# Optimization experiments

Hardware: AMD Instinct MI355X
Metric: run time of the kernel (lower is better)

## Reference

```python
import jax, jax.numpy as jnp
import numpy as np

T, E, H, V, K = 1024, 300, 512, 100000, 12
START, STOP = 10, 11


def setup_inputs() -> dict:
    key = jax.random.key(0)
    ks = jax.random.split(key, 12)
    s = 0.05
    sentence = jax.random.randint(ks[0], (T,), 0, V, dtype=jnp.int32)
    tags = jax.random.randint(ks[1], (T,), 0, START, dtype=jnp.int32)  # real tags only
    word_embeds = jax.random.normal(ks[2], (V, E), jnp.float32) * 0.1

    def lstm_p(k):
        k1, k2 = jax.random.split(k)
        return (jax.random.normal(k1, (4 * H, E), jnp.float32) * s,
                jax.random.normal(k2, (4 * H, H), jnp.float32) * s,
                jnp.zeros(4 * H, jnp.float32), jnp.zeros(4 * H, jnp.float32))

    Wih_f, Whh_f, bih_f, bhh_f = lstm_p(ks[3])
    Wih_b, Whh_b, bih_b, bhh_b = lstm_p(ks[4])
    D = 2 * H
    attn_W = jax.random.normal(ks[5], (D, D), jnp.float32) * s
    attn_b = jnp.zeros(D, jnp.float32)
    h2h1_W = jax.random.normal(ks[6], (D, 2 * D), jnp.float32) * s
    h2h1_b = jnp.zeros(D, jnp.float32)
    tag_W = jax.random.normal(ks[7], (K, D), jnp.float32) * s
    tag_b = jnp.zeros(K, jnp.float32)
    transitions = jax.random.normal(ks[8], (K, K), jnp.float32) * 0.01
    transitions = transitions.at[START, :].set(-10000.0).at[:, STOP].set(-10000.0)
    return dict(sentence=sentence, tags=tags, word_embeds=word_embeds,
                Wih_f=Wih_f, Whh_f=Whh_f, bih_f=bih_f, bhh_f=bhh_f,
                Wih_b=Wih_b, Whh_b=Whh_b, bih_b=bih_b, bhh_b=bhh_b,
                attn_W=attn_W, attn_b=attn_b, h2h1_W=h2h1_W, h2h1_b=h2h1_b,
                tag_W=tag_W, tag_b=tag_b, transitions=transitions)


def _lstm_pass(x, Wih, Whh, bih, bhh):
    # x: [T, E] -> hs: [T, H]   (PyTorch LSTM gate order i,f,g,o)
    xg = x @ Wih.T + bih  # [T, 4H] precomputed input contribution

    def step(carry, g_in):
        h, c = carry
        g = g_in + h @ Whh.T + bhh
        i, f, gg, o = jnp.split(g, 4)
        i = jax.nn.sigmoid(i); f = jax.nn.sigmoid(f)
        gg = jnp.tanh(gg); o = jax.nn.sigmoid(o)
        c = f * c + i * gg
        h = o * jnp.tanh(c)
        return (h, c), h

    init = (jnp.zeros(H, x.dtype), jnp.zeros(H, x.dtype))
    _, hs = jax.lax.scan(step, init, xg)
    return hs


def reference(sentence, tags, word_embeds, Wih_f, Whh_f, bih_f, bhh_f,
              Wih_b, Whh_b, bih_b, bhh_b, attn_W, attn_b,
              h2h1_W, h2h1_b, tag_W, tag_b, transitions):
    x = word_embeds[sentence]                       # [T, E]  (dropout is eval no-op)
    h_fwd = _lstm_pass(x, Wih_f, Whh_f, bih_f, bhh_f)
    h_bwd = _lstm_pass(x[::-1], Wih_b, Whh_b, bih_b, bhh_b)[::-1]
    enc = jnp.concatenate([h_fwd, h_bwd], axis=-1)  # [T, 2H]

    # Attn 'general': energy(t, i) = enc[t] . (W enc[i] + b); vectorized per-timestep loop
    proj = enc @ attn_W.T + attn_b                  # [T, 2H]
    scores = enc @ proj.T                           # [T, T]
    w = jax.nn.softmax(scores, axis=-1)
    ctx = w @ enc                                   # [T, 2H]

    h1 = jnp.tanh(jnp.concatenate([enc, ctx], axis=-1) @ h2h1_W.T + h2h1_b)  # [T, 2H]
    feats = h1 @ tag_W.T + tag_b                    # [T, K]

    # CRF forward algorithm (log partition); transitions[to, from]
    alpha0 = jnp.full((K,), -10000.0, feats.dtype).at[START].set(0.0)

    def crf_step(alpha, feat):
        a = jax.nn.logsumexp(alpha[None, :] + transitions, axis=1) + feat
        return a, None

    alpha, _ = jax.lax.scan(crf_step, alpha0, feats)
    logZ = jax.nn.logsumexp(alpha + transitions[STOP])

    # gold path score (_score_sentence)
    pad_start = jnp.concatenate([jnp.array([START], tags.dtype), tags])
    pad_stop = jnp.concatenate([tags, jnp.array([STOP], tags.dtype)])
    gold = transitions[pad_stop, pad_start].sum() + feats[jnp.arange(T), tags].sum()

    return logZ - gold  # CRF negative log-likelihood for this sentence
```

## Files before the change

kernel.cpp:

```cpp
#include <hip/hip_runtime.h>
#include <hip/hip_fp16.h>

#define T_LEN 1024
#define E_DIM 300
#define H_DIM 512
#define D_DIM 1024
#define K_TAGS 12
#define G4 2048

typedef __attribute__((ext_vector_type(8))) short short8x;
typedef __attribute__((ext_vector_type(4))) float f32x4;

static __device__ __forceinline__ float frcp(float x){ return __builtin_amdgcn_rcpf(x); }
static __device__ __forceinline__ float sigm(float x){ return frcp(1.f + __expf(-x)); }
static __device__ __forceinline__ float ftanh(float x){
  const float e = __expf(2.f * fabsf(x));
  const float t = 1.f - 2.f * frcp(e + 1.f);
  return copysignf(t, x);
}
static __device__ __forceinline__ unsigned short f2b(float f){
  unsigned u = __float_as_uint(f);
  return (unsigned short)((u + 0x7fffu + ((u >> 16) & 1u)) >> 16);
}
static __device__ __forceinline__ uint4 pack8(const float* s){
  uint4 o;
  o.x = (unsigned)f2b(s[0]) | ((unsigned)f2b(s[1]) << 16);
  o.y = (unsigned)f2b(s[2]) | ((unsigned)f2b(s[3]) << 16);
  o.z = (unsigned)f2b(s[4]) | ((unsigned)f2b(s[5]) << 16);
  o.w = (unsigned)f2b(s[6]) | ((unsigned)f2b(s[7]) << 16);
  return o;
}
static __device__ __forceinline__ uint4 pack8u(const unsigned short* s){
  uint4 o;
  o.x = (unsigned)s[0] | ((unsigned)s[1] << 16);
  o.y = (unsigned)s[2] | ((unsigned)s[3] << 16);
  o.z = (unsigned)s[4] | ((unsigned)s[5] << 16);
  o.w = (unsigned)s[6] | ((unsigned)s[7] << 16);
  return o;
}

__global__ void k_gather(const int* __restrict__ sent, const float* __restrict__ we,
                         unsigned short* __restrict__ xh){
  int idx = blockIdx.x*256 + threadIdx.x;
  if (idx < T_LEN*E_DIM){
    int t = idx / E_DIM, e = idx - t*E_DIM;
    xh[idx] = f2b(we[(size_t)sent[t]*E_DIM + e]);
  }
}

__global__ __launch_bounds__(256) void k_cast(const float* __restrict__ src,
                                              unsigned short* __restrict__ dst,
                                              int n4){
  int i = blockIdx.x*256 + threadIdx.x;
  if (i < n4){
    const float4 v = *reinterpret_cast<const float4*>(src + (size_t)i*4);
    ushort2 a, b;
    a.x = f2b(v.x); a.y = f2b(v.y); b.x = f2b(v.z); b.y = f2b(v.w);
    *reinterpret_cast<ushort2*>(dst + (size_t)i*4)     = a;
    *reinterpret_cast<ushort2*>(dst + (size_t)i*4 + 2) = b;
  }
}

__global__ void k_init(unsigned* __restrict__ hbuf, unsigned* __restrict__ rdy){
  int i = blockIdx.x*256 + threadIdx.x;
  if (i < 2048) hbuf[i] = 0u;
  if (i < 32)   rdy[i]  = 0u;
}

__global__ __launch_bounds__(256) void k_gemm_mfma(
    const unsigned short* __restrict__ Ah, int lda,
    const unsigned short* __restrict__ Bh, int ldb,
    const float* __restrict__ bias, int act,
    void* __restrict__ Cp, int ldc, int cbf16, int M, int N, int K)
{
  __shared__ __align__(16) unsigned short As[64*40];
  __shared__ __align__(16) unsigned short Bs[64*40];
  const int tid = threadIdx.x;
  const int bm = blockIdx.y*64, bn = blockIdx.x*64;
  const int r  = tid >> 2, c8 = (tid & 3) * 8;
  const int wave = tid >> 6, lane = tid & 63;
  const int wm = (wave >> 1) * 32, wn = (wave & 1) * 32;
  const int col = lane & 15, quad = lane >> 4;

  const unsigned short* arow = Ah + (size_t)(bm+r)*lda;
  const unsigned short* brow = Bh + (size_t)(bn+r)*ldb;

  uint4* aw = (uint4*)(As + r*40 + c8);
  uint4* bw = (uint4*)(Bs + r*40 + c8);

  f32x4 acc[2][2];
  #pragma unroll
  for (int i=0;i<2;i++)
    #pragma unroll
    for (int j=0;j<2;j++) acc[i][j] = (f32x4){0.f,0.f,0.f,0.f};

  for (int k0 = 0; k0 < K; k0 += 32){
    uint4 avv, bvv;
    if (k0 + 32 <= K){
      avv = *(const uint4*)(arow + k0 + c8);
      bvv = *(const uint4*)(brow + k0 + c8);
    } else {
      unsigned short ta[8], tb[8];
      #pragma unroll
      for (int i=0;i<8;i++){
        const int kk = k0 + c8 + i;
        ta[i] = (kk < K) ? arow[kk] : (unsigned short)0;
        tb[i] = (kk < K) ? brow[kk] : (unsigned short)0;
      }
      avv = pack8u(ta); bvv = pack8u(tb);
    }
    if (k0) __syncthreads();
    *aw = avv; *bw = bvv;
    __syncthreads();
    const short8x a0 = *(const short8x*)(As + (wm+col)*40    + quad*8);
    const short8x a1 = *(const short8x*)(As + (wm+16+col)*40 + quad*8);
    const short8x b0 = *(const short8x*)(Bs + (wn+col)*40    + quad*8);
    const short8x b1 = *(const short8x*)(Bs + (wn+16+col)*40 + quad*8);
    acc[0][0] = __builtin_amdgcn_mfma_f32_16x16x32_bf16(a0, b0, acc[0][0], 0, 0, 0);
    acc[0][1] = __builtin_amdgcn_mfma_f32_16x16x32_bf16(a0, b1, acc[0][1], 0, 0, 0);
    acc[1][0] = __builtin_amdgcn_mfma_f32_16x16x32_bf16(a1, b0, acc[1][0], 0, 0, 0);
    acc[1][1] = __builtin_amdgcn_mfma_f32_16x16x32_bf16(a1, b1, acc[1][1], 0, 0, 0);
  }

  #pragma unroll
  for (int mt=0;mt<2;mt++){
    #pragma unroll
    for (int nt=0;nt<2;nt++){
      const int cc = bn + wn + 16*nt + col;
      const float bs = bias ? bias[cc] : 0.f;
      #pragma unroll
      for (int i=0;i<4;i++){
        const int rr = bm + wm + 16*mt + quad*4 + i;
        float v = acc[mt][nt][i] + bs;
        if (act) v = ftanh(v);
        if (cbf16) ((unsigned short*)Cp)[(size_t)rr*ldc + cc] = f2b(v);
        else       ((float*)Cp)[(size_t)rr*ldc + cc] = v;
      }
    }
  }
}

__global__ __launch_bounds__(256, 1) void k_lstm_fused(
    const float* __restrict__ Whh_f, const float* __restrict__ Whh_b,
    const float* __restrict__ bih_f, const float* __restrict__ bhh_f,
    const float* __restrict__ bih_b, const float* __restrict__ bhh_b,
    float* __restrict__ xg_f, float* __restrict__ xg_b,
    const unsigned short* __restrict__ xh,
    const unsigned short* __restrict__ Wih_fh, const unsigned short* __restrict__ Wih_bh,
    unsigned* __restrict__ hbuf, unsigned* __restrict__ xgReady,
    float* __restrict__ enc)
{
  __shared__ __align__(16) unsigned short As[64*40];
  __shared__ __align__(16) unsigned short Bs[64*40];
  __shared__ __align__(16) unsigned short lds_hb[512];
  __shared__ __align__(16) float raw[64];

  const int tid = threadIdx.x;
  const int wave = tid >> 6, lane = tid & 63;
  const int col = lane & 15, quad = lane >> 4;

  if (blockIdx.x >= 64){
    const int pid = blockIdx.x - 64;
    const int r  = tid >> 2, c8 = (tid & 3) * 8;
    const int wm = (wave >> 1) * 32, wn = (wave & 1) * 32;
    uint4* aw = (uint4*)(As + r*40 + c8);
    uint4* bw = (uint4*)(Bs + r*40 + c8);

    for (int j = pid; j < 1024; j += 192){
      const int bm = j >> 6, rem = j & 63, pdir = rem >> 5, bn = rem & 31;
      const unsigned short* Bh = pdir ? Wih_bh : Wih_fh;
      float* C = pdir ? xg_b : xg_f;
      const int am = pdir ? (1023 - (bm*64 + r)) : (bm*64 + r);
      const unsigned short* arow = xh + (size_t)am*E_DIM;
      const unsigned short* brow = Bh + (size_t)(bn*64 + r)*E_DIM;

      f32x4 acc[2][2];
      #pragma unroll
      for (int i=0;i<2;i++)
        #pragma unroll
        for (int jj=0;jj<2;jj++) acc[i][jj] = (f32x4){0.f,0.f,0.f,0.f};

      for (int k0 = 0; k0 < E_DIM; k0 += 32){
        uint4 avv, bvv;
        if (k0 + 32 <= E_DIM){
          avv = *(const uint4*)(arow + k0 + c8);
          bvv = *(const uint4*)(brow + k0 + c8);
        } else {
          unsigned short ta[8], tb[8];
          #pragma unroll
          for (int i=0;i<8;i++){
            const int kk = k0 + c8 + i;
            ta[i] = (kk < E_DIM) ? arow[kk] : (unsigned short)0;
            tb[i] = (kk < E_DIM) ? brow[kk] : (unsigned short)0;
          }
          avv = pack8u(ta); bvv = pack8u(tb);
        }
        __syncthreads();
        *aw = avv; *bw = bvv;
        __syncthreads();
        const short8x a0 = *(const short8x*)(As + (wm+col)*40    + quad*8);
        const short8x a1 = *(const short8x*)(As + (wm+16+col)*40 + quad*8);
        const short8x b0 = *(const short8x*)(Bs + (wn+col)*40    + quad*8);
        const short8x b1 = *(const short8x*)(Bs + (wn+16+col)*40 + quad*8);
        acc[0][0] = __builtin_amdgcn_mfma_f32_16x16x32_bf16(a0, b0, acc[0][0], 0, 0, 0);
        acc[0][1] = __builtin_amdgcn_mfma_f32_16x16x32_bf16(a0, b1, acc[0][1], 0, 0, 0);
        acc[1][0] = __builtin_amdgcn_mfma_f32_16x16x32_bf16(a1, b0, acc[1][0], 0, 0, 0);
        acc[1][1] = __builtin_amdgcn_mfma_f32_16x16x32_bf16(a1, b1, acc[1][1], 0, 0, 0);
      }
      #pragma unroll
      for (int mt=0;mt<2;mt++)
        #pragma unroll
        for (int nt=0;nt<2;nt++)
          #pragma unroll
          for (int i=0;i<4;i++)
            C[(size_t)(bm*64 + wm + 16*mt + quad*4 + i)*G4 + (bn*64 + wn + 16*nt + col)]
              = acc[mt][nt][i];
      __syncthreads();
      if (tid == 0)
        __hip_atomic_fetch_add(&xgReady[pdir*16 + bm], 1u,
                               __ATOMIC_RELEASE, __HIP_MEMORY_SCOPE_AGENT);
    }
    return;
  }

  const int dir = blockIdx.x >> 5;
  const int w   = blockIdx.x & 31;

  const float* Whh = dir ? Whh_b : Whh_f;
  const float* xg  = dir ? xg_b  : xg_f;
  unsigned* rdy = xgReady + dir*16;

  const int rowA = wave*H_DIM + w*16 + col;
  short8x w_frag[16];
  #pragma unroll
  for (int s=0;s<16;s++){
    const float* bp = Whh + (size_t)rowA*H_DIM + s*32 + quad*8;
    uint4 u = pack8(bp);
    w_frag[s] = *reinterpret_cast<short8x*>(&u);
  }

  float bias_r = 0.f, xg_cur = 0.f, c_reg = 0.f;
  int row2 = 0, readyBlk = 0;
  if (tid < 64){
    row2 = (tid >> 4)*H_DIM + w*16 + (tid & 15);
    bias_r = dir ? (bih_b[row2] + bhh_b[row2]) : (bih_f[row2] + bhh_f[row2]);
    while (__hip_atomic_load(rdy, __ATOMIC_RELAXED, __HIP_MEMORY_SCOPE_AGENT) != 32u) {}
    (void)__hip_atomic_load(rdy, __ATOMIC_ACQUIRE, __HIP_MEMORY_SCOPE_AGENT);
    readyBlk = 1;
    xg_cur = xg[row2];
  }

  unsigned* hb = hbuf + dir*1024;

  for (int t = 1; t <= T_LEN; ++t){
    {
      unsigned* s0 = hb + ((t-1)&1)*512 + tid;
      const unsigned want = (unsigned)(t-1);
      unsigned v0 = __hip_atomic_load(s0,     __ATOMIC_RELAXED, __HIP_MEMORY_SCOPE_AGENT);
      unsigned v1 = __hip_atomic_load(s0+256, __ATOMIC_RELAXED, __HIP_MEMORY_SCOPE_AGENT);
      while (((v0 >> 16) != want) || ((v1 >> 16) != want)){
        v0 = __hip_atomic_load(s0,     __ATOMIC_RELAXED, __HIP_MEMORY_SCOPE_AGENT);
        v1 = __hip_atomic_load(s0+256, __ATOMIC_RELAXED, __HIP_MEMORY_SCOPE_AGENT);
      }
      lds_hb[tid]     = (unsigned short)(v0 & 0xffffu);
      lds_hb[tid+256] = (unsigned short)(v1 & 0xffffu);
    }
    __syncthreads();

    float xg_nxt = 0.f;
    if (tid < 64 && t < T_LEN){
      const int nb = t >> 6;
      if (nb >= readyBlk){
        while (__hip_atomic_load(rdy + nb, __ATOMIC_RELAXED, __HIP_MEMORY_SCOPE_AGENT) != 32u) {}
        (void)__hip_atomic_load(rdy + nb, __ATOMIC_ACQUIRE, __HIP_MEMORY_SCOPE_AGENT);
        readyBlk = nb + 1;
      }
      xg_nxt = xg[(size_t)t*G4 + row2];
    }

    f32x4 a0 = (f32x4){0.f,0.f,0.f,0.f}, a1 = (f32x4){0.f,0.f,0.f,0.f};
    #pragma unroll
    for (int s=0;s<16;s+=2){
      const short8x b0 = *(const short8x*)(lds_hb + s*32     + quad*8);
      const short8x b1 = *(const short8x*)(lds_hb + (s+1)*32 + quad*8);
      a0 = __builtin_amdgcn_mfma_f32_16x16x32_bf16(w_frag[s],   b0, a0, 0, 0, 0);
      a1 = __builtin_amdgcn_mfma_f32_16x16x32_bf16(w_frag[s+1], b1, a1, 0, 0, 0);
    }
    if (col == 0){
      f32x4 asum = a0 + a1;
      *reinterpret_cast<f32x4*>(raw + wave*16 + quad*4) = asum;
    }
    __syncthreads();

    if (tid < 64){
      float v = raw[tid] + bias_r + xg_cur;
      const float va = ((tid >> 4) == 2) ? ftanh(v) : sigm(v);
      const int l2 = tid & 15;
      const float iv = __shfl(va, l2);
      const float fv = __shfl(va, l2 + 16);
      const float gg = __shfl(va, l2 + 32);
      const float ov = __shfl(va, l2 + 48);
      if (tid < 16){
        c_reg = fv*c_reg + iv*gg;
        const float hh = ov*ftanh(c_reg);
        const int hj = w*16 + tid;
        const unsigned hv = ((unsigned)t << 16) | (unsigned)f2b(hh);
        __hip_atomic_store(hb + (t&1)*512 + hj, hv,
                           __ATOMIC_RELAXED, __HIP_MEMORY_SCOPE_AGENT);
        const int tt = dir ? (T_LEN - t) : (t - 1);
        enc[(size_t)tt*D_DIM + dir*H_DIM + hj] = hh;
      }
      xg_cur = xg_nxt;
    }
    __syncthreads();
  }
}

__global__ __launch_bounds__(256) void k_softmax(float* __restrict__ S,
                                                 unsigned short* __restrict__ Sh){
  float* r = S + (size_t)blockIdx.x*1024;
  unsigned short* rh = Sh + (size_t)blockIdx.x*1024;
  const int tid = threadIdx.x;
  float v[4];
  #pragma unroll
  for (int i=0;i<4;i++) v[i] = r[tid + i*256];
  float m = fmaxf(fmaxf(v[0],v[1]), fmaxf(v[2],v[3]));
  #pragma unroll
  for (int off=32; off>=1; off>>=1) m = fmaxf(m, __shfl_xor(m, off));
  __shared__ float red[4], red2[4];
  const int wid = tid >> 6, lane = tid & 63;
  if (lane == 0) red[wid] = m;
  __syncthreads();
  m = fmaxf(fmaxf(red[0],red[1]), fmaxf(red[2],red[3]));
  float s = 0.f;
  #pragma unroll
  for (int i=0;i<4;i++){ v[i] = __expf(v[i]-m); s += v[i]; }
  #pragma unroll
  for (int off=32; off>=1; off>>=1) s += __shfl_xor(s, off);
  if (lane == 0) red2[wid] = s;
  __syncthreads();
  s = red2[0]+red2[1]+red2[2]+red2[3];
  const float inv = frcp(s);
  #pragma unroll
  for (int i=0;i<4;i++){
    const float o = v[i]*inv;
    r[tid + i*256]  = o;
    rh[tid + i*256] = f2b(o);
  }
}

__global__ __launch_bounds__(256) void k_encprep(const float* __restrict__ src,
                                                 unsigned short* __restrict__ cath,
                                                 unsigned short* __restrict__ encT){
  __shared__ float tile[32][33];
  const int bx = blockIdx.x*32, by = blockIdx.y*32;
  const int tx = threadIdx.x & 31, ty8 = threadIdx.x >> 5;
  #pragma unroll
  for (int i=ty8;i<32;i+=8){
    const float v = src[(size_t)(by+i)*1024 + bx+tx];
    tile[i][tx] = v;
    cath[(size_t)(by+i)*2048 + bx+tx] = f2b(v);
  }
  __syncthreads();
  #pragma unroll
  for (int i=ty8;i<32;i+=8) encT[(size_t)(bx+i)*1024 + by+tx] = f2b(tile[tx][i]);
}

__global__ __launch_bounds__(256) void k_feats(
    const float* __restrict__ h1, const float* __restrict__ tagW,
    const float* __restrict__ tagb, float* __restrict__ feats)
{
  const int t = blockIdx.x;
  const int wave = threadIdx.x >> 6, lane = threadIdx.x & 63;
  const float* hr = h1 + (size_t)t*D_DIM;
  float hv[16];
  #pragma unroll
  for (int i=0;i<16;i++) hv[i] = hr[lane + 64*i];
  #pragma unroll
  for (int j=0;j<3;j++){
    const int tag = wave*3 + j;
    const float* wr = tagW + (size_t)tag*D_DIM;
    float s = 0.f;
    #pragma unroll
    for (int i=0;i<16;i++) s += hv[i]*wr[lane + 64*i];
    #pragma unroll
    for (int off=32; off>=1; off>>=1) s += __shfl_xor(s, off);
    if (lane == 0) feats[(size_t)t*K_TAGS + tag] = s + tagb[tag];
  }
}

__global__ __launch_bounds__(64) void k_crf1(const float* __restrict__ feats,
                                             const float* __restrict__ trans,
                                             float* __restrict__ chunkM){
  const int c = blockIdx.x;
  const int r = threadIdx.x;
  __shared__ float sT[144];
  __shared__ float sF[16*12];
  for (int i=r; i<144; i+=64) sT[i] = trans[i];
  const int t0 = c*16;
  for (int i=r; i<192; i+=64) sF[i] = feats[(size_t)t0*K_TAGS + i];
  __syncthreads();
  if (r < 12){
    float m[12], nm[12];
    #pragma unroll
    for (int k=0;k<12;k++) m[k] = sT[k*12 + r] + sF[k];
    for (int s=1; s<16; ++s){
      #pragma unroll
      for (int i=0;i<12;i++){
        float v[12]; float mx = -1e30f;
        #pragma unroll
        for (int k=0;k<12;k++){ v[k] = sT[i*12+k] + m[k]; mx = fmaxf(mx, v[k]); }
        float ss = 0.f;
        #pragma unroll
        for (int k=0;k<12;k++) ss += __expf(v[k]-mx);
        nm[i] = sF[s*12+i] + mx + __logf(ss);
      }
      #pragma unroll
      for (int i=0;i<12;i++) m[i] = nm[i];
    }
    #pragma unroll
    for (int k=0;k<12;k++) chunkM[c*144 + k*12 + r] = m[k];
  }
}

__global__ __launch_bounds__(128) void k_crf2(const float* __restrict__ chunkM,
                                              const float* __restrict__ feats,
                                              const float* __restrict__ trans,
                                              const int* __restrict__ tags,
                                              float* __restrict__ out){
  const int tid = threadIdx.x, wave = tid >> 6, lane = tid & 63;
  __shared__ float sGold;
  float alpha = (lane == 10) ? 0.f : -10000.f;
  if (wave == 1){
    float g = 0.f;
    for (int i = lane; i <= T_LEN; i += 64){
      const int to = (i < T_LEN) ? tags[i]   : 11;
      const int fr = (i == 0)    ? 10        : tags[i-1];
      g += trans[to*K_TAGS + fr];
      if (i < T_LEN) g += feats[(size_t)i*K_TAGS + tags[i]];
    }
    #pragma unroll
    for (int off=32; off>=1; off>>=1) g += __shfl_xor(g, off);
    if (lane == 0) sGold = g;
  } else {
    float pf[12];
    #pragma unroll
    for (int k=0;k<12;k++) pf[k] = (lane < 12) ? chunkM[lane*12 + k] : 0.f;
    for (int c=0; c<64; ++c){
      float av[12];
      #pragma unroll
      for (int j=0;j<12;j++) av[j] = __shfl(alpha, j);
      float cur[12];
      #pragma unroll
      for (int k=0;k<12;k++) cur[k] = pf[k];
      if (c+1 < 64){
        #pragma unroll
        for (int k=0;k<12;k++)
          pf[k] = (lane < 12) ? chunkM[(c+1)*144 + lane*12 + k] : 0.f;
      }
      if (lane < 12){
        float v[12]; float mx = -1e30f;
        #pragma unroll
        for (int k=0;k<12;k++){ v[k] = cur[k] + av[k]; mx = fmaxf(mx, v[k]); }
        float ss = 0.f;
        #pragma unroll
        for (int k=0;k<12;k++) ss += __expf(v[k]-mx);
        alpha = mx + __logf(ss);
      }
    }
  }
  __syncthreads();
  if (wave == 0){
    float v = (lane < K_TAGS) ? (alpha + trans[11*K_TAGS + lane]) : -1e30f;
    float m = v;
    #pragma unroll
    for (int off=32; off>=1; off>>=1) m = fmaxf(m, __shfl_xor(m, off));
    float e = (lane < K_TAGS) ? __expf(v - m) : 0.f;
    #pragma unroll
    for (int off=32; off>=1; off>>=1) e += __shfl_xor(e, off);
    if (lane == 0) out[0] = (m + __logf(e)) - sGold;
  }
}

extern "C" void kernel_launch(void* const* d_in, const int* in_sizes, int n_in,
                              void* d_out, int out_size, void* d_ws, size_t ws_size,
                              hipStream_t stream)
{
  const int*   sentence = (const int*)d_in[0];
  const int*   tags     = (const int*)d_in[1];
  const float* we       = (const float*)d_in[2];
  const float* Wih_f    = (const float*)d_in[3];
  const float* Whh_f    = (const float*)d_in[4];
  const float* bih_f    = (const float*)d_in[5];
  const float* bhh_f    = (const float*)d_in[6];
  const float* Wih_b    = (const float*)d_in[7];
  const float* Whh_b    = (const float*)d_in[8];
  const float* bih_b    = (const float*)d_in[9];
  const float* bhh_b    = (const float*)d_in[10];
  const float* attn_W   = (const float*)d_in[11];
  const float* attn_b   = (const float*)d_in[12];
  const float* h2h1_W   = (const float*)d_in[13];
  const float* h2h1_b   = (const float*)d_in[14];
  const float* tag_W    = (const float*)d_in[15];
  const float* tag_b    = (const float*)d_in[16];
  const float* trans    = (const float*)d_in[17];
  float* out = (float*)d_out;

  float* ws = (float*)d_ws;
  float* R1 = ws;
  float* R2 = ws + 2097152;
  float* R3 = ws + 4194304;
  float* R4 = ws + 5242880;
  float* feats = ws + 6291456;
  unsigned* hbuf = (unsigned*)(ws + 6303744);

  float* xg_f = R1;
  float* xg_b = R2;
  float* enc  = R3;
  unsigned short* xh      = (unsigned short*)R4;
  unsigned short* Wih_fh  = (unsigned short*)R4 + 307200;
  unsigned short* Wih_bh  = (unsigned short*)R4 + 921600;
  unsigned* xgReady = (unsigned*)feats;
  unsigned short* cath    = (unsigned short*)R1;
  unsigned short* attn_Wh = (unsigned short*)(R1 + 1048576);
  unsigned short* h2h1_Wh = (unsigned short*)R2;
  float* scores = R2 + 1048576;
  unsigned short* encT    = (unsigned short*)R4;
  unsigned short* projh   = (unsigned short*)R4 + 1048576;
  unsigned short* scoresh = (unsigned short*)R3;
  float* h1     = R3;
  float* chunkM = R4;

  k_gather<<<dim3((T_LEN*E_DIM + 255)/256), dim3(256), 0, stream>>>(sentence, we, xh);
  k_init<<<dim3(8), dim3(256), 0, stream>>>(hbuf, xgReady);
  k_cast<<<dim3(600),  dim3(256), 0, stream>>>(Wih_f, Wih_fh, 153600);
  k_cast<<<dim3(600),  dim3(256), 0, stream>>>(Wih_b, Wih_bh, 153600);
  k_lstm_fused<<<dim3(256), dim3(256), 0, stream>>>(Whh_f, Whh_b, bih_f, bhh_f,
      bih_b, bhh_b, xg_f, xg_b, xh, Wih_fh, Wih_bh, hbuf, xgReady, enc);
  k_encprep<<<dim3(32,32), dim3(256), 0, stream>>>(enc, cath, encT);
  k_cast<<<dim3(1024), dim3(256), 0, stream>>>(attn_W, attn_Wh, 262144);
  k_cast<<<dim3(2048), dim3(256), 0, stream>>>(h2h1_W, h2h1_Wh, 524288);
  k_gemm_mfma<<<dim3(16,16), dim3(256), 0, stream>>>(cath, 2048,
      attn_Wh, D_DIM, attn_b, 0, projh, D_DIM, 1, T_LEN, D_DIM, D_DIM);
  k_gemm_mfma<<<dim3(16,16), dim3(256), 0, stream>>>(cath, 2048,
      projh, D_DIM, nullptr, 0, scores, T_LEN, 0, T_LEN, T_LEN, D_DIM);
  k_softmax<<<dim3(1024), dim3(256), 0, stream>>>(scores, scoresh);
  k_gemm_mfma<<<dim3(16,16), dim3(256), 0, stream>>>(scoresh, T_LEN,
      encT, D_DIM, nullptr, 0, cath + 1024, 2048, 1, T_LEN, D_DIM, T_LEN);
  k_gemm_mfma<<<dim3(16,16), dim3(256), 0, stream>>>(cath, 2048,
      h2h1_Wh, 2048, h2h1_b, 1, h1, D_DIM, 0, T_LEN, D_DIM, 2048);
  k_feats<<<dim3(1024), dim3(256), 0, stream>>>(h1, tag_W, tag_b, feats);
  k_crf1<<<dim3(64), dim3(64), 0, stream>>>(feats, trans, chunkM);
  k_crf2<<<dim3(1), dim3(128), 0, stream>>>(chunkM, feats, trans, tags, out);
}
```

Baseline: 1.823 ms.

## Fuse post-LSTM stages into one persistent kernel with grid barriers

The separate gather, cast and init kernels become one pre-pass kernel. All post-LSTM kernels (enc transpose and cast, weight casts, four GEMMs, softmax, tag features, both CRF stages) are merged into one 256-block persistent kernel that uses atomic grid barriers between phases. Barrier counters reuse hbuf, which the LSTM kernel's block 0 resets to zero at the end. This removes about ten kernel launches and their inter-kernel gaps, at the cost of spin-wait barriers and a correctness dependency on all 256 blocks being co-resident.

```diff
diff --git a/kernel.cpp b/kernel.cpp
--- a/kernel.cpp
+++ b/kernel.cpp
@@ -39,104 +39,31 @@
   return o;
 }
 
-__global__ void k_gather(const int* __restrict__ sent, const float* __restrict__ we,
-                         unsigned short* __restrict__ xh){
-  int idx = blockIdx.x*256 + threadIdx.x;
-  if (idx < T_LEN*E_DIM){
-    int t = idx / E_DIM, e = idx - t*E_DIM;
-    xh[idx] = f2b(we[(size_t)sent[t]*E_DIM + e]);
-  }
-}
-
-__global__ __launch_bounds__(256) void k_cast(const float* __restrict__ src,
-                                              unsigned short* __restrict__ dst,
-                                              int n4){
-  int i = blockIdx.x*256 + threadIdx.x;
-  if (i < n4){
-    const float4 v = *reinterpret_cast<const float4*>(src + (size_t)i*4);
+__global__ __launch_bounds__(256) void k_pre(
+    const int* __restrict__ sent, const float* __restrict__ we,
+    unsigned short* __restrict__ xh,
+    const float* __restrict__ Wf, unsigned short* __restrict__ Wfh,
+    const float* __restrict__ Wb, unsigned short* __restrict__ Wbh,
+    unsigned* __restrict__ hbuf, unsigned* __restrict__ rdy)
+{
+  const int i = blockIdx.x*256 + threadIdx.x;
+  if (i < 2048) hbuf[i] = 0u;
+  else if (i < 2080) rdy[i-2048] = 0u;
+  for (int g = i; g < T_LEN*E_DIM; g += 600*256){
+    int t = g / E_DIM, e = g - t*E_DIM;
+    xh[g] = f2b(we[(size_t)sent[t]*E_DIM + e]);
+  }
+  if (i < 153600){
+    const float4 v = *reinterpret_cast<const float4*>(Wf + (size_t)i*4);
     ushort2 a, b;
     a.x = f2b(v.x); a.y = f2b(v.y); b.x = f2b(v.z); b.y = f2b(v.w);
-    *reinterpret_cast<ushort2*>(dst + (size_t)i*4)     = a;
-    *reinterpret_cast<ushort2*>(dst + (size_t)i*4 + 2) = b;
-  }
-}
-
-__global__ void k_init(unsigned* __restrict__ hbuf, unsigned* __restrict__ rdy){
-  int i = blockIdx.x*256 + threadIdx.x;
-  if (i < 2048) hbuf[i] = 0u;
-  if (i < 32)   rdy[i]  = 0u;
-}
-
-__global__ __launch_bounds__(256) void k_gemm_mfma(
-    const unsigned short* __restrict__ Ah, int lda,
-    const unsigned short* __restrict__ Bh, int ldb,
-    const float* __restrict__ bias, int act,
-    void* __restrict__ Cp, int ldc, int cbf16, int M, int N, int K)
-{
-  __shared__ __align__(16) unsigned short As[64*40];
-  __shared__ __align__(16) unsigned short Bs[64*40];
-  const int tid = threadIdx.x;
-  const int bm = blockIdx.y*64, bn = blockIdx.x*64;
-  const int r  = tid >> 2, c8 = (tid & 3) * 8;
-  const int wave = tid >> 6, lane = tid & 63;
-  const int wm = (wave >> 1) * 32, wn = (wave & 1) * 32;
-  const int col = lane & 15, quad = lane >> 4;
-
-  const unsigned short* arow = Ah + (size_t)(bm+r)*lda;
-  const unsigned short* brow = Bh + (size_t)(bn+r)*ldb;
-
-  uint4* aw = (uint4*)(As + r*40 + c8);
-  uint4* bw = (uint4*)(Bs + r*40 + c8);
-
-  f32x4 acc[2][2];
-  #pragma unroll
-  for (int i=0;i<2;i++)
-    #pragma unroll
-    for (int j=0;j<2;j++) acc[i][j] = (f32x4){0.f,0.f,0.f,0.f};
-
-  for (int k0 = 0; k0 < K; k0 += 32){
-    uint4 avv, bvv;
-    if (k0 + 32 <= K){
-      avv = *(const uint4*)(arow + k0 + c8);
-      bvv = *(const uint4*)(brow + k0 + c8);
-    } else {
-      unsigned short ta[8], tb[8];
-      #pragma unroll
-      for (int i=0;i<8;i++){
-        const int kk = k0 + c8 + i;
-        ta[i] = (kk < K) ? arow[kk] : (unsigned short)0;
-        tb[i] = (kk < K) ? brow[kk] : (unsigned short)0;
-      }
-      avv = pack8u(ta); bvv = pack8u(tb);
-    }
-    if (k0) __syncthreads();
-    *aw = avv; *bw = bvv;
-    __syncthreads();
-    const short8x a0 = *(const short8x*)(As + (wm+col)*40    + quad*8);
-    const short8x a1 = *(const short8x*)(As + (wm+16+col)*40 + quad*8);
-    const short8x b0 = *(const short8x*)(Bs + (wn+col)*40    + quad*8);
-    const short8x b1 = *(const short8x*)(Bs + (wn+16+col)*40 + quad*8);
-    acc[0][0] = __builtin_amdgcn_mfma_f32_16x16x32_bf16(a0, b0, acc[0][0], 0, 0, 0);
-    acc[0][1] = __builtin_amdgcn_mfma_f32_16x16x32_bf16(a0, b1, acc[0][1], 0, 0, 0);
-    acc[1][0] = __builtin_amdgcn_mfma_f32_16x16x32_bf16(a1, b0, acc[1][0], 0, 0, 0);
-    acc[1][1] = __builtin_amdgcn_mfma_f32_16x16x32_bf16(a1, b1, acc[1][1], 0, 0, 0);
-  }
-
-  #pragma unroll
-  for (int mt=0;mt<2;mt++){
-    #pragma unroll
-    for (int nt=0;nt<2;nt++){
-      const int cc = bn + wn + 16*nt + col;
-      const float bs = bias ? bias[cc] : 0.f;
-      #pragma unroll
-      for (int i=0;i<4;i++){
-        const int rr = bm + wm + 16*mt + quad*4 + i;
-        float v = acc[mt][nt][i] + bs;
-        if (act) v = ftanh(v);
-        if (cbf16) ((unsigned short*)Cp)[(size_t)rr*ldc + cc] = f2b(v);
-        else       ((float*)Cp)[(size_t)rr*ldc + cc] = v;
-      }
-    }
+    *reinterpret_cast<ushort2*>(Wfh + (size_t)i*4)     = a;
+    *reinterpret_cast<ushort2*>(Wfh + (size_t)i*4 + 2) = b;
+    const float4 u = *reinterpret_cast<const float4*>(Wb + (size_t)i*4);
+    ushort2 c, d;
+    c.x = f2b(u.x); c.y = f2b(u.y); d.x = f2b(u.z); d.y = f2b(u.w);
+    *reinterpret_cast<ushort2*>(Wbh + (size_t)i*4)     = c;
+    *reinterpret_cast<ushort2*>(Wbh + (size_t)i*4 + 2) = d;
   }
 }
 
@@ -314,171 +241,278 @@
     }
     __syncthreads();
   }
-}
-
-__global__ __launch_bounds__(256) void k_softmax(float* __restrict__ S,
-                                                 unsigned short* __restrict__ Sh){
-  float* r = S + (size_t)blockIdx.x*1024;
-  unsigned short* rh = Sh + (size_t)blockIdx.x*1024;
+
+  if (blockIdx.x == 0 && tid < 16)
+    __hip_atomic_store(hbuf + tid, 0u, __ATOMIC_RELAXED, __HIP_MEMORY_SCOPE_AGENT);
+}
+
+static __device__ __forceinline__ void gbar(unsigned* c){
+  __syncthreads();
+  if (threadIdx.x == 0){
+    __hip_atomic_fetch_add(c, 1u, __ATOMIC_RELEASE, __HIP_MEMORY_SCOPE_AGENT);
+    while (__hip_atomic_load(c, __ATOMIC_RELAXED, __HIP_MEMORY_SCOPE_AGENT) != 256u) {}
+    (void)__hip_atomic_load(c, __ATOMIC_ACQUIRE, __HIP_MEMORY_SCOPE_AGENT);
+  }
+  __syncthreads();
+}
+
+static __device__ void gemm_tile(
+    const unsigned short* __restrict__ Ah, int lda,
+    const unsigned short* __restrict__ Bh, int ldb,
+    const float* __restrict__ bias, int act,
+    void* __restrict__ Cp, int ldc, int cbf16, int K, int bm, int bn,
+    unsigned short* As, unsigned short* Bs)
+{
   const int tid = threadIdx.x;
-  float v[4];
+  const int r  = tid >> 2, c8 = (tid & 3) * 8;
+  const int wave = tid >> 6, lane = tid & 63;
+  const int wm = (wave >> 1) * 32, wn = (wave & 1) * 32;
+  const int col = lane & 15, quad = lane >> 4;
+
+  const unsigned short* arow = Ah + (size_t)(bm+r)*lda;
+  const unsigned short* brow = Bh + (size_t)(bn+r)*ldb;
+  uint4* aw = (uint4*)(As + r*40 + c8);
+  uint4* bw = (uint4*)(Bs + r*40 + c8);
+
+  f32x4 acc[2][2];
   #pragma unroll
-  for (int i=0;i<4;i++) v[i] = r[tid + i*256];
-  float m = fmaxf(fmaxf(v[0],v[1]), fmaxf(v[2],v[3]));
+  for (int i=0;i<2;i++)
+    #pragma unroll
+    for (int j=0;j<2;j++) acc[i][j] = (f32x4){0.f,0.f,0.f,0.f};
+
+  for (int k0 = 0; k0 < K; k0 += 32){
+    const uint4 avv = *(const uint4*)(arow + k0 + c8);
+    const uint4 bvv = *(const uint4*)(brow + k0 + c8);
+    __syncthreads();
+    *aw = avv; *bw = bvv;
+    __syncthreads();
+    const short8x a0 = *(const short8x*)(As + (wm+col)*40    + quad*8);
+    const short8x a1 = *(const short8x*)(As + (wm+16+col)*40 + quad*8);
+    const short8x b0 = *(const short8x*)(Bs + (wn+col)*40    + quad*8);
+    const short8x b1 = *(const short8x*)(Bs + (wn+16+col)*40 + quad*8);
+    acc[0][0] = __builtin_amdgcn_mfma_f32_16x16x32_bf16(a0, b0, acc[0][0], 0, 0, 0);
+    acc[0][1] = __builtin_amdgcn_mfma_f32_16x16x32_bf16(a0, b1, acc[0][1], 0, 0, 0);
+    acc[1][0] = __builtin_amdgcn_mfma_f32_16x16x32_bf16(a1, b0, acc[1][0], 0, 0, 0);
+    acc[1][1] = __builtin_amdgcn_mfma_f32_16x16x32_bf16(a1, b1, acc[1][1], 0, 0, 0);
+  }
+
   #pragma unroll
-  for (int off=32; off>=1; off>>=1) m = fmaxf(m, __shfl_xor(m, off));
+  for (int mt=0;mt<2;mt++){
+    #pragma unroll
+    for (int nt=0;nt<2;nt++){
+      const int cc = bn + wn + 16*nt + col;
+      const float bs = bias ? bias[cc] : 0.f;
+      #pragma unroll
+      for (int i=0;i<4;i++){
+        const int rr = bm + wm + 16*mt + quad*4 + i;
+        float v = acc[mt][nt][i] + bs;
+        if (act) v = ftanh(v);
+        if (cbf16) ((unsigned short*)Cp)[(size_t)rr*ldc + cc] = f2b(v);
+        else       ((float*)Cp)[(size_t)rr*ldc + cc] = v;
+      }
+    }
+  }
+}
+
+__global__ __launch_bounds__(256, 1) void k_tail(
+    const float* __restrict__ enc,
+    unsigned short* __restrict__ cath, unsigned short* __restrict__ encT,
+    const float* __restrict__ attn_W, unsigned short* __restrict__ attn_Wh,
+    const float* __restrict__ attn_b,
+    const float* __restrict__ h2h1_W, unsigned short* __restrict__ h2h1_Wh,
+    const float* __restrict__ h2h1_b,
+    unsigned short* __restrict__ projh, float* __restrict__ scores,
+    unsigned short* __restrict__ scoresh, float* __restrict__ h1,
+    const float* __restrict__ tagW, const float* __restrict__ tagb,
+    float* __restrict__ feats, const float* __restrict__ trans,
+    const int* __restrict__ tags, float* __restrict__ chunkM,
+    unsigned* __restrict__ bars, float* __restrict__ out)
+{
+  __shared__ __align__(16) unsigned short As[64*40];
+  __shared__ __align__(16) unsigned short Bs[64*40];
   __shared__ float red[4], red2[4];
-  const int wid = tid >> 6, lane = tid & 63;
-  if (lane == 0) red[wid] = m;
-  __syncthreads();
-  m = fmaxf(fmaxf(red[0],red[1]), fmaxf(red[2],red[3]));
-  float s = 0.f;
-  #pragma unroll
-  for (int i=0;i<4;i++){ v[i] = __expf(v[i]-m); s += v[i]; }
-  #pragma unroll
-  for (int off=32; off>=1; off>>=1) s += __shfl_xor(s, off);
-  if (lane == 0) red2[wid] = s;
-  __syncthreads();
-  s = red2[0]+red2[1]+red2[2]+red2[3];
-  const float inv = frcp(s);
-  #pragma unroll
-  for (int i=0;i<4;i++){
-    const float o = v[i]*inv;
-    r[tid + i*256]  = o;
-    rh[tid + i*256] = f2b(o);
-  }
-}
-
-__global__ __launch_bounds__(256) void k_encprep(const float* __restrict__ src,
-                                                 unsigned short* __restrict__ cath,
-                                                 unsigned short* __restrict__ encT){
-  __shared__ float tile[32][33];
-  const int bx = blockIdx.x*32, by = blockIdx.y*32;
-  const int tx = threadIdx.x & 31, ty8 = threadIdx.x >> 5;
-  #pragma unroll
-  for (int i=ty8;i<32;i+=8){
-    const float v = src[(size_t)(by+i)*1024 + bx+tx];
-    tile[i][tx] = v;
-    cath[(size_t)(by+i)*2048 + bx+tx] = f2b(v);
-  }
-  __syncthreads();
-  #pragma unroll
-  for (int i=ty8;i<32;i+=8) encT[(size_t)(bx+i)*1024 + by+tx] = f2b(tile[tx][i]);
-}
-
-__global__ __launch_bounds__(256) void k_feats(
-    const float* __restrict__ h1, const float* __restrict__ tagW,
-    const float* __restrict__ tagb, float* __restrict__ feats)
-{
-  const int t = blockIdx.x;
-  const int wave = threadIdx.x >> 6, lane = threadIdx.x & 63;
-  const float* hr = h1 + (size_t)t*D_DIM;
-  float hv[16];
-  #pragma unroll
-  for (int i=0;i<16;i++) hv[i] = hr[lane + 64*i];
-  #pragma unroll
-  for (int j=0;j<3;j++){
-    const int tag = wave*3 + j;
-    const float* wr = tagW + (size_t)tag*D_DIM;
+  const int tid = threadIdx.x, b = blockIdx.x;
+  const int wave = tid >> 6, lane = tid & 63;
+  const int bm = (b >> 4) * 64, bn = (b & 15) * 64;
+
+  {
+    float (*tile)[33] = (float(*)[33])As;
+    const int tx = tid & 31, ty8 = tid >> 5;
+    for (int j = b; j < 1024; j += 256){
+      const int bx = (j & 31)*32, by = (j >> 5)*32;
+      __syncthreads();
+      #pragma unroll
+      for (int i=ty8;i<32;i+=8){
+        const float v = enc[(size_t)(by+i)*1024 + bx+tx];
+        tile[i][tx] = v;
+        cath[(size_t)(by+i)*2048 + bx+tx] = f2b(v);
+      }
+      __syncthreads();
+      #pragma unroll
+      for (int i=ty8;i<32;i+=8) encT[(size_t)(bx+i)*1024 + by+tx] = f2b(tile[tx][i]);
+    }
+    const int gid = b*256 + tid;
+    for (int c = gid; c < 262144; c += 65536){
+      const float4 v = *reinterpret_cast<const float4*>(attn_W + (size_t)c*4);
+      ushort2 x, y; x.x=f2b(v.x); x.y=f2b(v.y); y.x=f2b(v.z); y.y=f2b(v.w);
+      *reinterpret_cast<ushort2*>(attn_Wh + (size_t)c*4)     = x;
+      *reinterpret_cast<ushort2*>(attn_Wh + (size_t)c*4 + 2) = y;
+    }
+    for (int c = gid; c < 524288; c += 65536){
+      const float4 v = *reinterpret_cast<const float4*>(h2h1_W + (size_t)c*4);
+      ushort2 x, y; x.x=f2b(v.x); x.y=f2b(v.y); y.x=f2b(v.z); y.y=f2b(v.w);
+      *reinterpret_cast<ushort2*>(h2h1_Wh + (size_t)c*4)     = x;
+      *reinterpret_cast<ushort2*>(h2h1_Wh + (size_t)c*4 + 2) = y;
+    }
+  }
+  gbar(bars + 0);
+
+  gemm_tile(cath, 2048, attn_Wh, D_DIM, attn_b, 0, projh, D_DIM, 1, D_DIM, bm, bn, As, Bs);
+  gbar(bars + 1);
+
+  gemm_tile(cath, 2048, projh, D_DIM, nullptr, 0, scores, T_LEN, 0, D_DIM, bm, bn, As, Bs);
+  gbar(bars + 2);
+
+  for (int rr = 0; rr < 4; ++rr){
+    float* r = scores + (size_t)(b*4 + rr)*1024;
+    unsigned short* rh = scoresh + (size_t)(b*4 + rr)*1024;
+    float v[4];
+    #pragma unroll
+    for (int i=0;i<4;i++) v[i] = r[tid + i*256];
+    float m = fmaxf(fmaxf(v[0],v[1]), fmaxf(v[2],v[3]));
+    #pragma unroll
+    for (int off=32; off>=1; off>>=1) m = fmaxf(m, __shfl_xor(m, off));
+    if (lane == 0) red[wave] = m;
+    __syncthreads();
+    m = fmaxf(fmaxf(red[0],red[1]), fmaxf(red[2],red[3]));
     float s = 0.f;
     #pragma unroll
-    for (int i=0;i<16;i++) s += hv[i]*wr[lane + 64*i];
+    for (int i=0;i<4;i++){ v[i] = __expf(v[i]-m); s += v[i]; }
     #pragma unroll
     for (int off=32; off>=1; off>>=1) s += __shfl_xor(s, off);
-    if (lane == 0) feats[(size_t)t*K_TAGS + tag] = s + tagb[tag];
-  }
-}
-
-__global__ __launch_bounds__(64) void k_crf1(const float* __restrict__ feats,
-                                             const float* __restrict__ trans,
-                                             float* __restrict__ chunkM){
-  const int c = blockIdx.x;
-  const int r = threadIdx.x;
-  __shared__ float sT[144];
-  __shared__ float sF[16*12];
-  for (int i=r; i<144; i+=64) sT[i] = trans[i];
-  const int t0 = c*16;
-  for (int i=r; i<192; i+=64) sF[i] = feats[(size_t)t0*K_TAGS + i];
-  __syncthreads();
-  if (r < 12){
-    float m[12], nm[12];
-    #pragma unroll
-    for (int k=0;k<12;k++) m[k] = sT[k*12 + r] + sF[k];
-    for (int s=1; s<16; ++s){
-      #pragma unroll
-      for (int i=0;i<12;i++){
-        float v[12]; float mx = -1e30f;
+    if (lane == 0) red2[wave] = s;
+    __syncthreads();
+    s = red2[0]+red2[1]+red2[2]+red2[3];
+    const float inv = frcp(s);
+    #pragma unroll
+    for (int i=0;i<4;i++){
+      const float o = v[i]*inv;
+      r[tid + i*256]  = o;
+      rh[tid + i*256] = f2b(o);
+    }
+    __syncthreads();
+  }
+  gbar(bars + 3);
+
+  gemm_tile(scoresh, T_LEN, encT, D_DIM, nullptr, 0, cath + 1024, 2048, 1, T_LEN, bm, bn, As, Bs);
+  gbar(bars + 4);
+
+  gemm_tile(cath, 2048, h2h1_Wh, 2048, h2h1_b, 1, h1, D_DIM, 0, 2048, bm, bn, As, Bs);
+  gbar(bars + 5);
+
+  for (int j = 0; j < 4; ++j){
+    const int t = b*4 + j;
+    const float* hr = h1 + (size_t)t*D_DIM;
+    float hv[16];
+    #pragma unroll
+    for (int i=0;i<16;i++) hv[i] = hr[lane + 64*i];
+    #pragma unroll
+    for (int jj=0;jj<3;jj++){
+      const int tag = wave*3 + jj;
+      const float* wr = tagW + (size_t)tag*D_DIM;
+      float s = 0.f;
+      #pragma unroll
+      for (int i=0;i<16;i++) s += hv[i]*wr[lane + 64*i];
+      #pragma unroll
+      for (int off=32; off>=1; off>>=1) s += __shfl_xor(s, off);
+      if (lane == 0) feats[(size_t)t*K_TAGS + tag] = s + tagb[tag];
+    }
+  }
+  gbar(bars + 6);
+
+  if (b < 64){
+    float* sT = (float*)Bs;
+    float* sF = sT + 144;
+    for (int q = tid; q < 144; q += 256) sT[q] = trans[q];
+    const int t0 = b*16;
+    for (int q = tid; q < 192; q += 256) sF[q] = feats[(size_t)t0*K_TAGS + q];
+    __syncthreads();
+    if (tid < 12){
+      const int r = tid;
+      float m[12], nm[12];
+      #pragma unroll
+      for (int k=0;k<12;k++) m[k] = sT[k*12 + r] + sF[k];
+      for (int s=1; s<16; ++s){
         #pragma unroll
-        for (int k=0;k<12;k++){ v[k] = sT[i*12+k] + m[k]; mx = fmaxf(mx, v[k]); }
-        float ss = 0.f;
+        for (int i=0;i<12;i++){
+          float v[12]; float mx = -1e30f;
+          #pragma unroll
+          for (int k=0;k<12;k++){ v[k] = sT[i*12+k] + m[k]; mx = fmaxf(mx, v[k]); }
+          float ss = 0.f;
+          #pragma unroll
+          for (int k=0;k<12;k++) ss += __expf(v[k]-mx);
+          nm[i] = sF[s*12+i] + mx + __logf(ss);
+        }
         #pragma unroll
-        for (int k=0;k<12;k++) ss += __expf(v[k]-mx);
-        nm[i] = sF[s*12+i] + mx + __logf(ss);
-      }
-      #pragma unroll
-      for (int i=0;i<12;i++) m[i] = nm[i];
-    }
-    #pragma unroll
-    for (int k=0;k<12;k++) chunkM[c*144 + k*12 + r] = m[k];
-  }
-}
-
-__global__ __launch_bounds__(128) void k_crf2(const float* __restrict__ chunkM,
-                                              const float* __restrict__ feats,
-                                              const float* __restrict__ trans,
-                                              const int* __restrict__ tags,
-                                              float* __restrict__ out){
-  const int tid = threadIdx.x, wave = tid >> 6, lane = tid & 63;
-  __shared__ float sGold;
-  float alpha = (lane == 10) ? 0.f : -10000.f;
-  if (wave == 1){
-    float g = 0.f;
-    for (int i = lane; i <= T_LEN; i += 64){
-      const int to = (i < T_LEN) ? tags[i]   : 11;
-      const int fr = (i == 0)    ? 10        : tags[i-1];
-      g += trans[to*K_TAGS + fr];
-      if (i < T_LEN) g += feats[(size_t)i*K_TAGS + tags[i]];
-    }
-    #pragma unroll
-    for (int off=32; off>=1; off>>=1) g += __shfl_xor(g, off);
-    if (lane == 0) sGold = g;
-  } else {
-    float pf[12];
-    #pragma unroll
-    for (int k=0;k<12;k++) pf[k] = (lane < 12) ? chunkM[lane*12 + k] : 0.f;
-    for (int c=0; c<64; ++c){
-      float av[12];
-      #pragma unroll
-      for (int j=0;j<12;j++) av[j] = __shfl(alpha, j);
-      float cur[12];
-      #pragma unroll
-      for (int k=0;k<12;k++) cur[k] = pf[k];
-      if (c+1 < 64){
+        for (int i=0;i<12;i++) m[i] = nm[i];
+      }
+      #pragma unroll
+      for (int k=0;k<12;k++) chunkM[b*144 + k*12 + r] = m[k];
+    }
+  }
+  gbar(bars + 7);
+
+  if (b == 0){
+    float alpha = (lane == 10) ? 0.f : -10000.f;
+    if (wave == 1){
+      float g = 0.f;
+      for (int i = lane; i <= T_LEN; i += 64){
+        const int to = (i < T_LEN) ? tags[i]   : 11;
+        const int fr = (i == 0)    ? 10        : tags[i-1];
+        g += trans[to*K_TAGS + fr];
+        if (i < T_LEN) g += feats[(size_t)i*K_TAGS + tags[i]];
+      }
+      #pragma unroll
+      for (int off=32; off>=1; off>>=1) g += __shfl_xor(g, off);
+      if (lane == 0) red[0] = g;
+    } else if (wave == 0){
+      float pf[12];
+      #pragma unroll
+      for (int k=0;k<12;k++) pf[k] = (lane < 12) ? chunkM[lane*12 + k] : 0.f;
+      for (int c=0; c<64; ++c){
+        float av[12];
         #pragma unroll
-        for (int k=0;k<12;k++)
-          pf[k] = (lane < 12) ? chunkM[(c+1)*144 + lane*12 + k] : 0.f;
-      }
-      if (lane < 12){
-        float v[12]; float mx = -1e30f;
+        for (int j=0;j<12;j++) av[j] = __shfl(alpha, j);
+        float cur[12];
         #pragma unroll
-        for (int k=0;k<12;k++){ v[k] = cur[k] + av[k]; mx = fmaxf(mx, v[k]); }
-        float ss = 0.f;
-        #pragma unroll
-        for (int k=0;k<12;k++) ss += __expf(v[k]-mx);
-        alpha = mx + __logf(ss);
-      }
-    }
-  }
-  __syncthreads();
-  if (wave == 0){
-    float v = (lane < K_TAGS) ? (alpha + trans[11*K_TAGS + lane]) : -1e30f;
-    float m = v;
-    #pragma unroll
-    for (int off=32; off>=1; off>>=1) m = fmaxf(m, __shfl_xor(m, off));
-    float e = (lane < K_TAGS) ? __expf(v - m) : 0.f;
-    #pragma unroll
-    for (int off=32; off>=1; off>>=1) e += __shfl_xor(e, off);
-    if (lane == 0) out[0] = (m + __logf(e)) - sGold;
+        for (int k=0;k<12;k++) cur[k] = pf[k];
+        if (c+1 < 64){
+          #pragma unroll
+          for (int k=0;k<12;k++)
+            pf[k] = (lane < 12) ? chunkM[(c+1)*144 + lane*12 + k] : 0.f;
+        }
+        if (lane < 12){
+          float v[12]; float mx = -1e30f;
+          #pragma unroll
+          for (int k=0;k<12;k++){ v[k] = cur[k] + av[k]; mx = fmaxf(mx, v[k]); }
+          float ss = 0.f;
+          #pragma unroll
+          for (int k=0;k<12;k++) ss += __expf(v[k]-mx);
+          alpha = mx + __logf(ss);
+        }
+      }
+    }
+    __syncthreads();
+    if (wave == 0){
+      float v = (lane < K_TAGS) ? (alpha + trans[11*K_TAGS + lane]) : -1e30f;
+      float m = v;
+      #pragma unroll
+      for (int off=32; off>=1; off>>=1) m = fmaxf(m, __shfl_xor(m, off));
+      float e = (lane < K_TAGS) ? __expf(v - m) : 0.f;
+      #pragma unroll
+      for (int off=32; off>=1; off>>=1) e += __shfl_xor(e, off);
+      if (lane == 0) out[0] = (m + __logf(e)) - red[0];
+    }
   }
 }
 
@@ -531,25 +565,12 @@
   float* h1     = R3;
   float* chunkM = R4;
 
-  k_gather<<<dim3((T_LEN*E_DIM + 255)/256), dim3(256), 0, stream>>>(sentence, we, xh);
-  k_init<<<dim3(8), dim3(256), 0, stream>>>(hbuf, xgReady);
-  k_cast<<<dim3(600),  dim3(256), 0, stream>>>(Wih_f, Wih_fh, 153600);
-  k_cast<<<dim3(600),  dim3(256), 0, stream>>>(Wih_b, Wih_bh, 153600);
+  k_pre<<<dim3(600), dim3(256), 0, stream>>>(sentence, we, xh,
+      Wih_f, Wih_fh, Wih_b, Wih_bh, hbuf, xgReady);
   k_lstm_fused<<<dim3(256), dim3(256), 0, stream>>>(Whh_f, Whh_b, bih_f, bhh_f,
       bih_b, bhh_b, xg_f, xg_b, xh, Wih_fh, Wih_bh, hbuf, xgReady, enc);
-  k_encprep<<<dim3(32,32), dim3(256), 0, stream>>>(enc, cath, encT);
-  k_cast<<<dim3(1024), dim3(256), 0, stream>>>(attn_W, attn_Wh, 262144);
-  k_cast<<<dim3(2048), dim3(256), 0, stream>>>(h2h1_W, h2h1_Wh, 524288);
-  k_gemm_mfma<<<dim3(16,16), dim3(256), 0, stream>>>(cath, 2048,
-      attn_Wh, D_DIM, attn_b, 0, projh, D_DIM, 1, T_LEN, D_DIM, D_DIM);
-  k_gemm_mfma<<<dim3(16,16), dim3(256), 0, stream>>>(cath, 2048,
-      projh, D_DIM, nullptr, 0, scores, T_LEN, 0, T_LEN, T_LEN, D_DIM);
-  k_softmax<<<dim3(1024), dim3(256), 0, stream>>>(scores, scoresh);
-  k_gemm_mfma<<<dim3(16,16), dim3(256), 0, stream>>>(scoresh, T_LEN,
-      encT, D_DIM, nullptr, 0, cath + 1024, 2048, 1, T_LEN, D_DIM, T_LEN);
-  k_gemm_mfma<<<dim3(16,16), dim3(256), 0, stream>>>(cath, 2048,
-      h2h1_Wh, 2048, h2h1_b, 1, h1, D_DIM, 0, T_LEN, D_DIM, 2048);
-  k_feats<<<dim3(1024), dim3(256), 0, stream>>>(h1, tag_W, tag_b, feats);
-  k_crf1<<<dim3(64), dim3(64), 0, stream>>>(feats, trans, chunkM);
-  k_crf2<<<dim3(1), dim3(128), 0, stream>>>(chunkM, feats, trans, tags, out);
-}
+  k_tail<<<dim3(256), dim3(256), 0, stream>>>(enc, cath, encT,
+      attn_W, attn_Wh, attn_b, h2h1_W, h2h1_Wh, h2h1_b,
+      projh, scores, scoresh, h1, tag_W, tag_b, feats, trans, tags,
+      chunkM, hbuf, out);
+}
```

Result: slower. 1.906 ms (+4.5%).
